# Optimization experiments

Measured on AMD Instinct MI355X. Metric: run time of the kernel, lower is better.

Reference implementation:

```python
import jax, jax.numpy as jnp
import numpy as np

B, S, D = 2, 2048, 1024
H, KVH = 16, 4
HD = D // H            # 64
REP = H // KVH         # 4
SCALE = HD ** -0.5


def setup_inputs() -> dict:
    key = jax.random.key(0)
    ks = jax.random.split(key, 5)
    x = jax.random.normal(ks[0], (B, S, D), dtype=jnp.float32)
    mask = jnp.ones((B, S), dtype=jnp.int32)
    # torch Linear weights: [out_features, in_features], y = x @ W.T
    Wq = jax.random.normal(ks[1], (D, D), dtype=jnp.float32) * (D ** -0.5)
    Wk = jax.random.normal(ks[2], (KVH * HD, D), dtype=jnp.float32) * (D ** -0.5)
    Wv = jax.random.normal(ks[3], (KVH * HD, D), dtype=jnp.float32) * (D ** -0.5)
    Wo = jax.random.normal(ks[4], (D, D), dtype=jnp.float32) * (D ** -0.5)
    return {"x": x, "mask": mask, "Wq": Wq, "Wk": Wk, "Wv": Wv, "Wo": Wo}


def reference(x, mask, Wq, Wk, Wv, Wo):
    b, s, _ = x.shape
    q = (x @ Wq.T).reshape(b, s, H, HD)          # [B,S,H,HD]
    k = (x @ Wk.T).reshape(b, s, KVH, HD)        # [B,S,KVH,HD]
    v = (x @ Wv.T).reshape(b, s, KVH, HD)
    # repeat_interleave along head dim: each kv head repeated REP times
    k = jnp.repeat(k, REP, axis=2)               # [B,S,H,HD]
    v = jnp.repeat(v, REP, axis=2)
    q = q.transpose(0, 2, 1, 3)                  # [B,H,S,HD]
    k = k.transpose(0, 2, 1, 3)
    v = v.transpose(0, 2, 1, 3)
    scores = jnp.einsum('bhqd,bhkd->bhqk', q, k) * SCALE  # [B,H,S,S]
    m = mask[:, None, None, :]                   # [B,1,1,S]
    scores = jnp.where(m == 0, jnp.float32(-jnp.inf), scores)
    attn = jax.nn.softmax(scores, axis=-1)
    out = jnp.einsum('bhqk,bhkd->bhqd', attn, v) # [B,H,S,HD]
    out = out.transpose(0, 2, 1, 3).reshape(b, s, D)
    return out @ Wo.T
```

## Files before the change

### kernel.cpp

```cpp
#include <hip/hip_runtime.h>
#include <hip/hip_bf16.h>
#include <stdint.h>

#define B_    2
#define S_    2048
#define D_    1024
#define H_    16
#define KVH_  4
#define HD_   64
#define REP_  4
#define BS_   (B_ * S_)
#define KVD_  256
#define QKVS_ 1536
#define NT_   (S_ / 64)

typedef unsigned short u16;
typedef short s16x4 __attribute__((ext_vector_type(4)));
typedef short s16x8 __attribute__((ext_vector_type(8)));
typedef float f32x4 __attribute__((ext_vector_type(4)));

typedef const __attribute__((address_space(1))) void* gvp;
typedef __attribute__((address_space(3))) void* lvp;

#define MFMA16(a, b, c) __builtin_amdgcn_mfma_f32_16x16x32_bf16((a), (b), (c), 0, 0, 0)

__device__ __forceinline__ u16 f2b(float f) {
  uint32_t u = __float_as_uint(f);
  u += 0x7fffu + ((u >> 16) & 1u);
  return (u16)(u >> 16);
}

__device__ __forceinline__ int swz64(int row, int slot) {
  return slot ^ (row & 7) ^ ((row >> 3) & 7);
}

#define N0_ (BS_ * D_ / 4)
#define N1_ (D_ * D_ / 4)
#define N2_ (KVD_ * D_ / 4)
__global__ void cvt5_kernel(const float* __restrict__ s0, const float* __restrict__ s1,
                            const float* __restrict__ s2, const float* __restrict__ s3,
                            const float* __restrict__ s4, u16* __restrict__ dst, int n4tot) {
  for (int i = blockIdx.x * blockDim.x + threadIdx.x; i < n4tot;
       i += gridDim.x * blockDim.x) {
    const float* src;
    int j = i;
    if (j < N0_) src = s0;
    else if ((j -= N0_) < N1_) src = s1;
    else if ((j -= N1_) < N2_) src = s2;
    else if ((j -= N2_) < N2_) src = s3;
    else { j -= N2_; src = s4; }
    const float4 v = reinterpret_cast<const float4*>(src)[j];
    uint2 o;
    o.x = (uint32_t)f2b(v.x) | ((uint32_t)f2b(v.y) << 16);
    o.y = (uint32_t)f2b(v.z) | ((uint32_t)f2b(v.w) << 16);
    reinterpret_cast<uint2*>(dst)[i] = o;
  }
}

template <int OUT_BF16>
__global__ __launch_bounds__(256) void gemm64(const u16* __restrict__ A,
                                              const u16* __restrict__ Bw,
                                              void* __restrict__ Cout,
                                              int M, int N, int K) {
  __shared__ u16 As[64 * 32];
  __shared__ u16 Bs[128 * 32];
  const int tid = threadIdx.x;
  const int lane = tid & 63;
  const int wid = tid >> 6;
  const int l16 = lane & 15;
  const int kq = lane >> 4;
  const int bm = blockIdx.y * 64;
  const int bn = blockIdx.x * 128;
  const int wr = (wid >> 1) * 32;
  const int wc = (wid & 1) * 64;

  f32x4 acc[2][4] = {};

  for (int kt = 0; kt < K; kt += 32) {
    __syncthreads();
    {
      const int e = tid * 8;
      const int row = e >> 5;
      const int col = e & 31;
      __builtin_amdgcn_global_load_lds((gvp)(A + (size_t)(bm + row) * K + kt + col),
                                       (lvp)(&As[e]), 16, 0, 0);
    }
#pragma unroll
    for (int i = 0; i < 2; ++i) {
      const int e = (i * 256 + tid) * 8;
      const int row = e >> 5;
      const int col = e & 31;
      __builtin_amdgcn_global_load_lds((gvp)(Bw + (size_t)(bn + row) * K + kt + col),
                                       (lvp)(&Bs[e]), 16, 0, 0);
    }
    __syncthreads();

    s16x8 af[2], bfr[4];
#pragma unroll
    for (int m = 0; m < 2; ++m)
      af[m] = *reinterpret_cast<const s16x8*>(&As[(wr + m * 16 + l16) * 32 + kq * 8]);
#pragma unroll
    for (int n = 0; n < 4; ++n)
      bfr[n] = *reinterpret_cast<const s16x8*>(&Bs[(wc + n * 16 + l16) * 32 + kq * 8]);
#pragma unroll
    for (int m = 0; m < 2; ++m)
#pragma unroll
      for (int n = 0; n < 4; ++n)
        acc[m][n] = MFMA16(af[m], bfr[n], acc[m][n]);
  }

#pragma unroll
  for (int m = 0; m < 2; ++m) {
    const int row0 = bm + wr + m * 16 + kq * 4;
#pragma unroll
    for (int n = 0; n < 4; ++n) {
      const int col = bn + wc + n * 16 + l16;
#pragma unroll
      for (int r = 0; r < 4; ++r) {
        if (OUT_BF16) {
          ((u16*)Cout)[(size_t)(row0 + r) * N + col] = f2b(acc[m][n][r]);
        } else {
          ((float*)Cout)[(size_t)(row0 + r) * N + col] = acc[m][n][r];
        }
      }
    }
  }
}

__global__ __launch_bounds__(256) void vtrans_kernel(const u16* __restrict__ QKV,
                                                     u16* __restrict__ VT) {
  __shared__ u16 T[64][72];
  const int tid = threadIdx.x;
  const int s0 = blockIdx.x * 64;
  const int bg = blockIdx.y;
  const int b = bg >> 2;
  const int g = bg & 3;
  const int r = tid >> 2;
  const int c0 = (tid & 3) * 16;
  const u16* src = QKV + (size_t)(b * S_ + s0 + r) * QKVS_ + D_ + KVD_ + g * HD_ + c0;
  const uint4 a = reinterpret_cast<const uint4*>(src)[0];
  const uint4 bq = reinterpret_cast<const uint4*>(src)[1];
  *reinterpret_cast<uint4*>(&T[r][c0]) = a;
  *reinterpret_cast<uint4*>(&T[r][c0 + 8]) = bq;
  __syncthreads();
  const int d = tid >> 2;
  u16 tmp[16];
#pragma unroll
  for (int j = 0; j < 16; ++j) tmp[j] = T[c0 + j][d];
  u16* dst = VT + ((size_t)bg * 64 + d) * S_ + s0 + c0;
  *reinterpret_cast<uint4*>(dst) = *reinterpret_cast<const uint4*>(&tmp[0]);
  *reinterpret_cast<uint4*>(dst + 8) = *reinterpret_cast<const uint4*>(&tmp[8]);
}

__global__ __launch_bounds__(256) void attn_kernel(const u16* __restrict__ QKV,
                                                   const u16* __restrict__ VT,
                                                   const int* __restrict__ mask,
                                                   u16* __restrict__ O) {
  __shared__ u16 Ks[2][64 * 64];
  __shared__ u16 Vt[2][64 * 64];

  const int tid = threadIdx.x;
  const int lane = tid & 63;
  const int wid = tid >> 6;
  const int l16 = lane & 15;
  const int kq = lane >> 4;
  const int bg = blockIdx.y;
  const int b = bg >> 2;
  const int g = bg & 3;
  const int h = g * REP_ + wid;
  const int q0 = blockIdx.x * 32;
  const u16* kv_base = QKV + (size_t)b * S_ * QKVS_ + D_ + g * HD_;
  const u16* vt_base = VT + (size_t)bg * 64 * S_;
  const int* maskp = mask + b * S_ + lane;
  const float Cs = 0.18033688011112042f;

  int koff[4][2];
#pragma unroll
  for (int n = 0; n < 4; ++n)
#pragma unroll
    for (int c = 0; c < 2; ++c) {
      const int row = n * 16 + l16;
      koff[n][c] = row * 64 + swz64(row, c * 4 + kq) * 8;
    }
  const int hs = kq >> 1;
  const int bo = 4 * (kq & 1);
  int voff[4][4];
#pragma unroll
  for (int m = 0; m < 4; ++m) {
    const int drow = m * 16 + l16;
    voff[m][0] = drow * 64 + swz64(drow, hs) * 8 + bo;
    voff[m][1] = drow * 64 + swz64(drow, 2 + hs) * 8 + bo;
    voff[m][2] = drow * 64 + swz64(drow, 4 + hs) * 8 + bo;
    voff[m][3] = drow * 64 + swz64(drow, 6 + hs) * 8 + bo;
  }
  int kst_src[2], vst_src[2], st_dst[2];
#pragma unroll
  for (int i = 0; i < 2; ++i) {
    const int e = (i * 256 + tid) * 8;
    const int row = e >> 6;
    const int slot = (e >> 3) & 7;
    st_dst[i] = e;
    kst_src[i] = row * QKVS_ + swz64(row, slot) * 8;
    vst_src[i] = row * S_ + swz64(row, slot) * 8;
  }

  auto kstage = [&](int buf, int kv0) {
#pragma unroll
    for (int i = 0; i < 2; ++i)
      __builtin_amdgcn_global_load_lds(
          (gvp)(kv_base + (size_t)kv0 * QKVS_ + kst_src[i]),
          (lvp)(&Ks[buf][st_dst[i]]), 16, 0, 0);
  };
  auto vstage = [&](int buf, int kv0) {
#pragma unroll
    for (int i = 0; i < 2; ++i)
      __builtin_amdgcn_global_load_lds(
          (gvp)(vt_base + kv0 + vst_src[i]),
          (lvp)(&Vt[buf][st_dst[i]]), 16, 0, 0);
  };

  s16x8 qf[2][2];
#pragma unroll
  for (int g2 = 0; g2 < 2; ++g2) {
    const u16* qp = QKV + (size_t)(b * S_ + q0 + g2 * 16 + l16) * QKVS_ + h * HD_ + kq * 8;
    qf[g2][0] = *reinterpret_cast<const s16x8*>(qp);
    qf[g2][1] = *reinterpret_cast<const s16x8*>(qp + 32);
  }

  kstage(0, 0);
  vstage(0, 0);
  int mcur = maskp[0];

  float m_run[2] = {-1e30f, -1e30f}, l_run[2] = {0.f, 0.f};
  f32x4 acc[2][4] = {};

#define ATTN_TILE(T_, BUF_)                                                       \
  {                                                                               \
    const int t_ = (T_);                                                          \
    __syncthreads();                                                              \
    const bool pfch = (t_ + 1 < NT_);                                             \
    int mnext = 0;                                                                \
    if (pfch) {                                                                   \
      kstage((BUF_) ^ 1, (t_ + 1) * 64);                                          \
      vstage((BUF_) ^ 1, (t_ + 1) * 64);                                          \
      mnext = maskp[(t_ + 1) * 64];                                               \
    }                                                                             \
    const u16* ks = &Ks[(BUF_)][0];                                               \
    const u16* vt = &Vt[(BUF_)][0];                                               \
    s16x8 kfr[4][2];                                                              \
    _Pragma("unroll") for (int n = 0; n < 4; ++n) {                               \
      kfr[n][0] = *reinterpret_cast<const s16x8*>(ks + koff[n][0]);               \
      kfr[n][1] = *reinterpret_cast<const s16x8*>(ks + koff[n][1]);               \
    }                                                                             \
    f32x4 sc[2][4];                                                               \
    __builtin_amdgcn_s_setprio(1);                                                \
    _Pragma("unroll") for (int n = 0; n < 4; ++n) {                               \
      f32x4 s0 = {0.f, 0.f, 0.f, 0.f};                                            \
      f32x4 s1 = {0.f, 0.f, 0.f, 0.f};                                            \
      s0 = MFMA16(kfr[n][0], qf[0][0], s0);                                       \
      s1 = MFMA16(kfr[n][0], qf[1][0], s1);                                       \
      s0 = MFMA16(kfr[n][1], qf[0][1], s0);                                       \
      s1 = MFMA16(kfr[n][1], qf[1][1], s1);                                       \
      sc[0][n] = s0;                                                              \
      sc[1][n] = s1;                                                              \
    }                                                                             \
    __builtin_amdgcn_s_setprio(0);                                                \
    const unsigned long long mbits = __ballot(mcur != 0);                         \
    if (~mbits) {                                                                 \
      _Pragma("unroll") for (int n = 0; n < 4; ++n)                               \
      _Pragma("unroll") for (int r = 0; r < 4; ++r) {                             \
        if (!((mbits >> (n * 16 + kq * 4 + r)) & 1ull)) {                         \
          sc[0][n][r] = -3.0e38f;                                                 \
          sc[1][n][r] = -3.0e38f;                                                 \
        }                                                                         \
      }                                                                           \
    }                                                                             \
    union PK { uint32_t u[8]; s16x8 v[2]; } pk[2];                                \
    _Pragma("unroll") for (int g2 = 0; g2 < 2; ++g2) {                            \
      float tm = -1e30f;                                                          \
      _Pragma("unroll") for (int n = 0; n < 4; ++n)                               \
      _Pragma("unroll") for (int r = 0; r < 4; ++r)                               \
          tm = fmaxf(tm, sc[g2][n][r]);                                           \
      tm = fmaxf(tm, __shfl_xor(tm, 16));                                         \
      tm = fmaxf(tm, __shfl_xor(tm, 32));                                         \
      if (!__all(tm <= m_run[g2] + 44.0f)) {                                      \
        const float mnew = fmaxf(m_run[g2], tm);                                  \
        const float fac = exp2f((m_run[g2] - mnew) * Cs);                         \
        m_run[g2] = mnew;                                                         \
        l_run[g2] *= fac;                                                         \
        _Pragma("unroll") for (int m = 0; m < 4; ++m)                             \
        _Pragma("unroll") for (int r = 0; r < 4; ++r) acc[g2][m][r] *= fac;       \
      }                                                                           \
      float rs = 0.f;                                                             \
      const float mneg = -m_run[g2] * Cs;                                         \
      _Pragma("unroll") for (int n = 0; n < 4; ++n)                               \
      _Pragma("unroll") for (int r = 0; r < 4; ++r) {                             \
        const float p = exp2f(fmaf(sc[g2][n][r], Cs, mneg));                      \
        sc[g2][n][r] = p;                                                         \
        rs += p;                                                                  \
      }                                                                           \
      rs += __shfl_xor(rs, 16);                                                   \
      rs += __shfl_xor(rs, 32);                                                   \
      l_run[g2] += rs;                                                            \
      _Pragma("unroll") for (int n = 0; n < 4; ++n) {                             \
        asm("v_cvt_pk_bf16_f32 %0, %1, %2"                                        \
            : "=v"(pk[g2].u[2 * n]) : "v"(sc[g2][n][0]), "v"(sc[g2][n][1]));      \
        asm("v_cvt_pk_bf16_f32 %0, %1, %2"                                        \
            : "=v"(pk[g2].u[2 * n + 1]) : "v"(sc[g2][n][2]), "v"(sc[g2][n][3]));  \
      }                                                                           \
    }                                                                             \
    s16x8 vfr[4][2];                                                              \
    _Pragma("unroll") for (int m = 0; m < 4; ++m) {                               \
      union VF { s16x4 h[2]; s16x8 v; } va, vb;                                   \
      va.h[0] = *reinterpret_cast<const s16x4*>(vt + voff[m][0]);                 \
      va.h[1] = *reinterpret_cast<const s16x4*>(vt + voff[m][1]);                 \
      vb.h[0] = *reinterpret_cast<const s16x4*>(vt + voff[m][2]);                 \
      vb.h[1] = *reinterpret_cast<const s16x4*>(vt + voff[m][3]);                 \
      vfr[m][0] = va.v;                                                           \
      vfr[m][1] = vb.v;                                                           \
    }                                                                             \
    __builtin_amdgcn_s_setprio(1);                                                \
    _Pragma("unroll") for (int m = 0; m < 4; ++m) {                               \
      acc[0][m] = MFMA16(vfr[m][0], pk[0].v[0], acc[0][m]);                       \
      acc[1][m] = MFMA16(vfr[m][0], pk[1].v[0], acc[1][m]);                       \
      acc[0][m] = MFMA16(vfr[m][1], pk[0].v[1], acc[0][m]);                       \
      acc[1][m] = MFMA16(vfr[m][1], pk[1].v[1], acc[1][m]);                       \
    }                                                                             \
    __builtin_amdgcn_s_setprio(0);                                                \
    mcur = mnext;                                                                 \
  }

  for (int t = 0; t < NT_; t += 2) {
    ATTN_TILE(t, 0)
    ATTN_TILE(t + 1, 1)
  }
#undef ATTN_TILE

#pragma unroll
  for (int g2 = 0; g2 < 2; ++g2) {
    const float rl = 1.0f / l_run[g2];
    u16* op = O + (size_t)(b * S_ + q0 + g2 * 16 + l16) * D_ + h * HD_ + kq * 4;
#pragma unroll
    for (int m = 0; m < 4; ++m) {
      uint2 o;
      o.x = (uint32_t)f2b(acc[g2][m][0] * rl) | ((uint32_t)f2b(acc[g2][m][1] * rl) << 16);
      o.y = (uint32_t)f2b(acc[g2][m][2] * rl) | ((uint32_t)f2b(acc[g2][m][3] * rl) << 16);
      *reinterpret_cast<uint2*>(op + m * 16) = o;
    }
  }
}

extern "C" void kernel_launch(void* const* d_in, const int* in_sizes, int n_in,
                              void* d_out, int out_size, void* d_ws, size_t ws_size,
                              hipStream_t stream) {
  const float* x = (const float*)d_in[0];
  const int* mask = (const int*)d_in[1];
  const float* Wq = (const float*)d_in[2];
  const float* Wk = (const float*)d_in[3];
  const float* Wv = (const float*)d_in[4];
  const float* Wo = (const float*)d_in[5];

  char* w = (char*)d_ws;
  u16* xb = (u16*)w;    w += (size_t)BS_ * D_ * 2;
  u16* Wqkvb = (u16*)w; w += (size_t)QKVS_ * D_ * 2;
  u16* Wob = (u16*)w;   w += (size_t)D_ * D_ * 2;
  u16* QKVw = (u16*)w;  w += (size_t)BS_ * QKVS_ * 2;
  u16* VTw = (u16*)w;   w += (size_t)B_ * KVH_ * HD_ * S_ * 2;
  u16* AOw = (u16*)w;   w += (size_t)BS_ * D_ * 2;

  const int n4tot = (BS_ * D_ + QKVS_ * D_ + D_ * D_) / 4;
  cvt5_kernel<<<dim3(2048), dim3(256), 0, stream>>>(x, Wq, Wk, Wv, Wo, xb, n4tot);

  gemm64<1><<<dim3(QKVS_ / 128, BS_ / 64), dim3(256), 0, stream>>>(xb, Wqkvb, QKVw, BS_, QKVS_, D_);
  vtrans_kernel<<<dim3(S_ / 64, B_ * KVH_), dim3(256), 0, stream>>>(QKVw, VTw);
  attn_kernel<<<dim3(S_ / 32, B_ * KVH_), dim3(256), 0, stream>>>(QKVw, VTw, mask, AOw);
  gemm64<0><<<dim3(D_ / 128, BS_ / 64), dim3(256), 0, stream>>>(AOw, Wob, (float*)d_out, BS_, D_, D_);
}
```

Baseline: 134.2 us.

## Widen attention KV tile to 128 and remap GEMM block order

The attention kernel now processes 128 keys per tile instead of 64. This halves the number of barrier and softmax-rescale steps per query block, at the cost of twice the LDS (64KB for double-buffered K and V) and more registers, with launch bounds set to 2 blocks per CU. The V tile uses a new 128-wide swizzle and reads V fragments per output block, and the mask is loaded in two 64-key halves. Separately, the GEMM remaps its block IDs so that consecutive workgroups are spread across 8 groups, aiming at better cache locality or scheduler placement.

```diff
diff --git a/kernel.cpp b/kernel.cpp
--- a/kernel.cpp
+++ b/kernel.cpp
@@ -12,7 +12,7 @@
 #define BS_   (B_ * S_)
 #define KVD_  256
 #define QKVS_ 1536
-#define NT_   (S_ / 64)
+#define NTT_  (S_ / 128)
 
 typedef unsigned short u16;
 typedef short s16x4 __attribute__((ext_vector_type(4)));
@@ -32,6 +32,9 @@
 
 __device__ __forceinline__ int swz64(int row, int slot) {
   return slot ^ (row & 7) ^ ((row >> 3) & 7);
+}
+__device__ __forceinline__ int swz128(int row, int slot) {
+  return slot ^ (row & 15);
 }
 
 #define N0_ (BS_ * D_ / 4)
@@ -69,8 +72,11 @@
   const int wid = tid >> 6;
   const int l16 = lane & 15;
   const int kq = lane >> 4;
-  const int bm = blockIdx.y * 64;
-  const int bn = blockIdx.x * 128;
+  const int nwg = gridDim.x * gridDim.y;
+  const int bid0 = blockIdx.y * gridDim.x + blockIdx.x;
+  const int bid = (bid0 & 7) * (nwg >> 3) + (bid0 >> 3);
+  const int bm = (bid / gridDim.x) * 64;
+  const int bn = (bid % gridDim.x) * 128;
   const int wr = (wid >> 1) * 32;
   const int wc = (wid & 1) * 64;
 
@@ -152,12 +158,12 @@
   *reinterpret_cast<uint4*>(dst + 8) = *reinterpret_cast<const uint4*>(&tmp[8]);
 }
 
-__global__ __launch_bounds__(256) void attn_kernel(const u16* __restrict__ QKV,
-                                                   const u16* __restrict__ VT,
-                                                   const int* __restrict__ mask,
-                                                   u16* __restrict__ O) {
-  __shared__ u16 Ks[2][64 * 64];
-  __shared__ u16 Vt[2][64 * 64];
+__global__ __launch_bounds__(256, 2) void attn_kernel(const u16* __restrict__ QKV,
+                                                      const u16* __restrict__ VT,
+                                                      const int* __restrict__ mask,
+                                                      u16* __restrict__ O) {
+  __shared__ u16 Ks[2][128 * 64];
+  __shared__ u16 Vt[2][64 * 128];
 
   const int tid = threadIdx.x;
   const int lane = tid & 63;
@@ -174,9 +180,9 @@
   const int* maskp = mask + b * S_ + lane;
   const float Cs = 0.18033688011112042f;
 
-  int koff[4][2];
-#pragma unroll
-  for (int n = 0; n < 4; ++n)
+  int koff[8][2];
+#pragma unroll
+  for (int n = 0; n < 8; ++n)
 #pragma unroll
     for (int c = 0; c < 2; ++c) {
       const int row = n * 16 + l16;
@@ -184,36 +190,33 @@
     }
   const int hs = kq >> 1;
   const int bo = 4 * (kq & 1);
-  int voff[4][4];
-#pragma unroll
-  for (int m = 0; m < 4; ++m) {
-    const int drow = m * 16 + l16;
-    voff[m][0] = drow * 64 + swz64(drow, hs) * 8 + bo;
-    voff[m][1] = drow * 64 + swz64(drow, 2 + hs) * 8 + bo;
-    voff[m][2] = drow * 64 + swz64(drow, 4 + hs) * 8 + bo;
-    voff[m][3] = drow * 64 + swz64(drow, 6 + hs) * 8 + bo;
-  }
-  int kst_src[2], vst_src[2], st_dst[2];
-#pragma unroll
-  for (int i = 0; i < 2; ++i) {
+  int vbase[8];
+#pragma unroll
+  for (int c = 0; c < 4; ++c) {
+    vbase[2 * c] = l16 * 128 + swz128(l16, 4 * c + hs) * 8 + bo;
+    vbase[2 * c + 1] = l16 * 128 + swz128(l16, 4 * c + 2 + hs) * 8 + bo;
+  }
+  int kst_src[4], vst_src[4], st_dst[4];
+#pragma unroll
+  for (int i = 0; i < 4; ++i) {
     const int e = (i * 256 + tid) * 8;
-    const int row = e >> 6;
-    const int slot = (e >> 3) & 7;
     st_dst[i] = e;
-    kst_src[i] = row * QKVS_ + swz64(row, slot) * 8;
-    vst_src[i] = row * S_ + swz64(row, slot) * 8;
+    const int krow = e >> 6;
+    kst_src[i] = krow * QKVS_ + swz64(krow, (e >> 3) & 7) * 8;
+    const int vrow = e >> 7;
+    vst_src[i] = vrow * S_ + swz128(vrow, (e >> 3) & 15) * 8;
   }
 
   auto kstage = [&](int buf, int kv0) {
 #pragma unroll
-    for (int i = 0; i < 2; ++i)
+    for (int i = 0; i < 4; ++i)
       __builtin_amdgcn_global_load_lds(
           (gvp)(kv_base + (size_t)kv0 * QKVS_ + kst_src[i]),
           (lvp)(&Ks[buf][st_dst[i]]), 16, 0, 0);
   };
   auto vstage = [&](int buf, int kv0) {
 #pragma unroll
-    for (int i = 0; i < 2; ++i)
+    for (int i = 0; i < 4; ++i)
       __builtin_amdgcn_global_load_lds(
           (gvp)(vt_base + kv0 + vst_src[i]),
           (lvp)(&Vt[buf][st_dst[i]]), 16, 0, 0);
@@ -229,7 +232,8 @@
 
   kstage(0, 0);
   vstage(0, 0);
-  int mcur = maskp[0];
+  int mcur0 = maskp[0];
+  int mcur1 = maskp[64];
 
   float m_run[2] = {-1e30f, -1e30f}, l_run[2] = {0.f, 0.f};
   f32x4 acc[2][4] = {};
@@ -238,47 +242,49 @@
   {                                                                               \
     const int t_ = (T_);                                                          \
     __syncthreads();                                                              \
-    const bool pfch = (t_ + 1 < NT_);                                             \
-    int mnext = 0;                                                                \
+    const bool pfch = (t_ + 1 < NTT_);                                            \
+    int mnext0 = 0, mnext1 = 0;                                                   \
     if (pfch) {                                                                   \
-      kstage((BUF_) ^ 1, (t_ + 1) * 64);                                          \
-      vstage((BUF_) ^ 1, (t_ + 1) * 64);                                          \
-      mnext = maskp[(t_ + 1) * 64];                                               \
+      kstage((BUF_) ^ 1, (t_ + 1) * 128);                                         \
+      vstage((BUF_) ^ 1, (t_ + 1) * 128);                                         \
+      mnext0 = maskp[(t_ + 1) * 128];                                             \
+      mnext1 = maskp[(t_ + 1) * 128 + 64];                                        \
     }                                                                             \
     const u16* ks = &Ks[(BUF_)][0];                                               \
     const u16* vt = &Vt[(BUF_)][0];                                               \
-    s16x8 kfr[4][2];                                                              \
-    _Pragma("unroll") for (int n = 0; n < 4; ++n) {                               \
-      kfr[n][0] = *reinterpret_cast<const s16x8*>(ks + koff[n][0]);               \
-      kfr[n][1] = *reinterpret_cast<const s16x8*>(ks + koff[n][1]);               \
-    }                                                                             \
-    f32x4 sc[2][4];                                                               \
+    f32x4 sc[2][8];                                                               \
     __builtin_amdgcn_s_setprio(1);                                                \
-    _Pragma("unroll") for (int n = 0; n < 4; ++n) {                               \
+    _Pragma("unroll") for (int n = 0; n < 8; ++n) {                               \
+      const s16x8 kf0 = *reinterpret_cast<const s16x8*>(ks + koff[n][0]);         \
+      const s16x8 kf1 = *reinterpret_cast<const s16x8*>(ks + koff[n][1]);         \
       f32x4 s0 = {0.f, 0.f, 0.f, 0.f};                                            \
       f32x4 s1 = {0.f, 0.f, 0.f, 0.f};                                            \
-      s0 = MFMA16(kfr[n][0], qf[0][0], s0);                                       \
-      s1 = MFMA16(kfr[n][0], qf[1][0], s1);                                       \
-      s0 = MFMA16(kfr[n][1], qf[0][1], s0);                                       \
-      s1 = MFMA16(kfr[n][1], qf[1][1], s1);                                       \
+      s0 = MFMA16(kf0, qf[0][0], s0);                                             \
+      s1 = MFMA16(kf0, qf[1][0], s1);                                             \
+      s0 = MFMA16(kf1, qf[0][1], s0);                                             \
+      s1 = MFMA16(kf1, qf[1][1], s1);                                             \
       sc[0][n] = s0;                                                              \
       sc[1][n] = s1;                                                              \
     }                                                                             \
     __builtin_amdgcn_s_setprio(0);                                                \
-    const unsigned long long mbits = __ballot(mcur != 0);                         \
-    if (~mbits) {                                                                 \
-      _Pragma("unroll") for (int n = 0; n < 4; ++n)                               \
-      _Pragma("unroll") for (int r = 0; r < 4; ++r) {                             \
-        if (!((mbits >> (n * 16 + kq * 4 + r)) & 1ull)) {                         \
-          sc[0][n][r] = -3.0e38f;                                                 \
-          sc[1][n][r] = -3.0e38f;                                                 \
+    const unsigned long long mb0 = __ballot(mcur0 != 0);                          \
+    const unsigned long long mb1 = __ballot(mcur1 != 0);                          \
+    if ((~mb0) | (~mb1)) {                                                        \
+      _Pragma("unroll") for (int n = 0; n < 8; ++n) {                             \
+        const unsigned long long mb = (n < 4) ? mb0 : mb1;                        \
+        const int sh = (n & 3) * 16 + kq * 4;                                     \
+        _Pragma("unroll") for (int r = 0; r < 4; ++r) {                           \
+          if (!((mb >> (sh + r)) & 1ull)) {                                       \
+            sc[0][n][r] = -3.0e38f;                                               \
+            sc[1][n][r] = -3.0e38f;                                               \
+          }                                                                       \
         }                                                                         \
       }                                                                           \
     }                                                                             \
-    union PK { uint32_t u[8]; s16x8 v[2]; } pk[2];                                \
+    union PK { uint32_t u[16]; s16x8 v[4]; } pk[2];                               \
     _Pragma("unroll") for (int g2 = 0; g2 < 2; ++g2) {                            \
       float tm = -1e30f;                                                          \
-      _Pragma("unroll") for (int n = 0; n < 4; ++n)                               \
+      _Pragma("unroll") for (int n = 0; n < 8; ++n)                               \
       _Pragma("unroll") for (int r = 0; r < 4; ++r)                               \
           tm = fmaxf(tm, sc[g2][n][r]);                                           \
       tm = fmaxf(tm, __shfl_xor(tm, 16));                                         \
@@ -293,7 +299,7 @@
       }                                                                           \
       float rs = 0.f;                                                             \
       const float mneg = -m_run[g2] * Cs;                                         \
-      _Pragma("unroll") for (int n = 0; n < 4; ++n)                               \
+      _Pragma("unroll") for (int n = 0; n < 8; ++n)                               \
       _Pragma("unroll") for (int r = 0; r < 4; ++r) {                             \
         const float p = exp2f(fmaf(sc[g2][n][r], Cs, mneg));                      \
         sc[g2][n][r] = p;                                                         \
@@ -302,35 +308,34 @@
       rs += __shfl_xor(rs, 16);                                                   \
       rs += __shfl_xor(rs, 32);                                                   \
       l_run[g2] += rs;                                                            \
-      _Pragma("unroll") for (int n = 0; n < 4; ++n) {                             \
+      _Pragma("unroll") for (int n = 0; n < 8; ++n) {                             \
         asm("v_cvt_pk_bf16_f32 %0, %1, %2"                                        \
             : "=v"(pk[g2].u[2 * n]) : "v"(sc[g2][n][0]), "v"(sc[g2][n][1]));      \
         asm("v_cvt_pk_bf16_f32 %0, %1, %2"                                        \
-            : "=v"(pk[g2].u[2 * n + 1]) : "v"(sc[g2][n][2]), "v"(sc[g2][n][3]));  \
-      }                                                                           \
-    }                                                                             \
-    s16x8 vfr[4][2];                                                              \
+            : "=v"(pk[g2].u[2 * n + 1]) : "v"(sc[g2][n][2]), "v"(sc[g2][n][3])); \
+      }                                                                           \
+    }                                                                             \
     _Pragma("unroll") for (int m = 0; m < 4; ++m) {                               \
-      union VF { s16x4 h[2]; s16x8 v; } va, vb;                                   \
-      va.h[0] = *reinterpret_cast<const s16x4*>(vt + voff[m][0]);                 \
-      va.h[1] = *reinterpret_cast<const s16x4*>(vt + voff[m][1]);                 \
-      vb.h[0] = *reinterpret_cast<const s16x4*>(vt + voff[m][2]);                 \
-      vb.h[1] = *reinterpret_cast<const s16x4*>(vt + voff[m][3]);                 \
-      vfr[m][0] = va.v;                                                           \
-      vfr[m][1] = vb.v;                                                           \
-    }                                                                             \
-    __builtin_amdgcn_s_setprio(1);                                                \
-    _Pragma("unroll") for (int m = 0; m < 4; ++m) {                               \
-      acc[0][m] = MFMA16(vfr[m][0], pk[0].v[0], acc[0][m]);                       \
-      acc[1][m] = MFMA16(vfr[m][0], pk[1].v[0], acc[1][m]);                       \
-      acc[0][m] = MFMA16(vfr[m][1], pk[0].v[1], acc[0][m]);                       \
-      acc[1][m] = MFMA16(vfr[m][1], pk[1].v[1], acc[1][m]);                       \
-    }                                                                             \
-    __builtin_amdgcn_s_setprio(0);                                                \
-    mcur = mnext;                                                                 \
-  }
-
-  for (int t = 0; t < NT_; t += 2) {
+      const u16* vr = vt + m * 2048;                                              \
+      s16x8 vfr[4];                                                               \
+      _Pragma("unroll") for (int c = 0; c < 4; ++c) {                             \
+        union VF { s16x4 h[2]; s16x8 v; } vv;                                     \
+        vv.h[0] = *reinterpret_cast<const s16x4*>(vr + vbase[2 * c]);             \
+        vv.h[1] = *reinterpret_cast<const s16x4*>(vr + vbase[2 * c + 1]);         \
+        vfr[c] = vv.v;                                                            \
+      }                                                                           \
+      __builtin_amdgcn_s_setprio(1);                                              \
+      _Pragma("unroll") for (int c = 0; c < 4; ++c) {                             \
+        acc[0][m] = MFMA16(vfr[c], pk[0].v[c], acc[0][m]);                        \
+        acc[1][m] = MFMA16(vfr[c], pk[1].v[c], acc[1][m]);                        \
+      }                                                                           \
+      __builtin_amdgcn_s_setprio(0);                                              \
+    }                                                                             \
+    mcur0 = mnext0;                                                               \
+    mcur1 = mnext1;                                                               \
+  }
+
+  for (int t = 0; t < NTT_; t += 2) {
     ATTN_TILE(t, 0)
     ATTN_TILE(t + 1, 1)
   }
```

Result: faster. 127.6 us (-4.9%).
